# Optimization experiments

Hardware: AMD Instinct MI355X
Metric: run time of the kernel (lower is better)

## Reference

```python
import jax, jax.numpy as jnp
import numpy as np

EPS = 1e-5

def conv3(x, w, b):
    # 3x3 conv, stride 1, pad 1, NCHW/OIHW
    y = jax.lax.conv_general_dilated(x, w, (1, 1), ((1, 1), (1, 1)),
                                     dimension_numbers=('NCHW', 'OIHW', 'NCHW'))
    return y + b[None, :, None, None]

def positional_norm(x):
    # per-pixel channel-wise norm; torch .var() is unbiased (ddof=1)
    mean = jnp.mean(x, axis=1, keepdims=True)
    var = jnp.var(x, axis=1, keepdims=True, ddof=1)
    return (x - mean) / jnp.sqrt(var + EPS)

def bilinear_gather(x, py, px):
    # x: [B,C,H,W]; py/px: [B,K,H,W] absolute sample coords -> [B,C,K,H,W]
    B, C, H, W = x.shape
    K = py.shape[1]
    xf = x.reshape(B, C, H * W)
    y0 = jnp.floor(py).astype(jnp.int32)
    x0 = jnp.floor(px).astype(jnp.int32)
    wy = py - y0.astype(x.dtype)
    wx = px - x0.astype(x.dtype)

    def corner(yi, xi):
        valid = ((yi >= 0) & (yi < H) & (xi >= 0) & (xi < W)).astype(x.dtype)
        idx = (jnp.clip(yi, 0, H - 1) * W + jnp.clip(xi, 0, W - 1)).reshape(B, 1, K * H * W)
        v = jnp.take_along_axis(xf, idx, axis=2).reshape(B, C, K, H, W)
        return v * valid[:, None]

    out = ((1 - wy) * (1 - wx))[:, None] * corner(y0, x0)
    out = out + ((1 - wy) * wx)[:, None] * corner(y0, x0 + 1)
    out = out + (wy * (1 - wx))[:, None] * corner(y0 + 1, x0)
    out = out + (wy * wx)[:, None] * corner(y0 + 1, x0 + 1)
    return out

def dcn_v2(feat, cond, w_off, b_off, w_dcn, b_dcn):
    # DCNv2Pack: conv_offset(cond) -> (o1, o2, mask); modulated deformable 3x3 conv on feat
    B, C, H, W = feat.shape
    om = conv3(cond, w_off, b_off)                      # [B, 27, H, W]
    off = om[:, :18].reshape(B, 9, 2, H, W)             # (dy, dx) per kernel tap
    mask = jax.nn.sigmoid(om[:, 18:])                   # [B, 9, H, W]
    dy, dx = off[:, :, 0], off[:, :, 1]
    ki = jnp.repeat(jnp.arange(-1.0, 2.0, dtype=feat.dtype), 3)   # tap row offsets
    kj = jnp.tile(jnp.arange(-1.0, 2.0, dtype=feat.dtype), 3)     # tap col offsets
    hh = jnp.arange(H, dtype=feat.dtype)
    ww = jnp.arange(W, dtype=feat.dtype)
    py = dy + hh[None, None, :, None] + ki[None, :, None, None]
    px = dx + ww[None, None, None, :] + kj[None, :, None, None]
    sampled = bilinear_gather(feat, py, px)             # [B,C,9,H,W]
    wk = w_dcn.reshape(w_dcn.shape[0], C, 9)
    out = jnp.einsum('bkhw,bckhw,ock->bohw', mask, sampled, wk)
    return out + b_dcn[None, :, None, None]

def spade_forward(x, ref, w1, b1, w2, b2, w_off, b_off, w_dcn, b_dcn, w_g, b_g, w_be, b_be):
    normalized = positional_norm(x)
    h = jax.nn.relu(conv3(jnp.concatenate((normalized, ref), axis=1), w1, b1))
    cond = jax.nn.relu(conv3(h, w2, b2))
    ref_refine = dcn_v2(ref, cond, w_off, b_off, w_dcn, b_dcn)
    gamma = conv3(ref_refine, w_g, b_g)
    beta = conv3(ref_refine, w_be, b_be)
    return normalized * (1 + gamma) + beta

def setup_inputs() -> dict:
    key = jax.random.key(0)
    ks = jax.random.split(key, 16)
    B, NC, SC, H, W = 2, 64, 64, 96, 96
    mid = (NC + SC) // 8  # 16
    s = 0.05
    inp = {
        'x': jax.random.normal(ks[0], (B, NC, H, W), jnp.float32),
        'ref': jax.random.normal(ks[1], (B, SC, H, W), jnp.float32),
        'w1': jax.random.normal(ks[2], (mid, NC + SC, 3, 3), jnp.float32) * s,
        'b1': jax.random.normal(ks[3], (mid,), jnp.float32) * s,
        'w2': jax.random.normal(ks[4], (SC, mid, 3, 3), jnp.float32) * s,
        'b2': jax.random.normal(ks[5], (SC,), jnp.float32) * s,
        'w_off': jax.random.normal(ks[6], (27, SC, 3, 3), jnp.float32) * 0.01,
        'b_off': jax.random.normal(ks[7], (27,), jnp.float32) * 0.01,
        'w_dcn': jax.random.normal(ks[8], (SC, SC, 3, 3), jnp.float32) * s,
        'b_dcn': jax.random.normal(ks[9], (SC,), jnp.float32) * s,
        'w_g': jax.random.normal(ks[10], (NC, SC, 3, 3), jnp.float32) * s,
        'b_g': jax.random.normal(ks[11], (NC,), jnp.float32) * s,
        'w_be': jax.random.normal(ks[12], (NC, SC, 3, 3), jnp.float32) * s,
        'b_be': jax.random.normal(ks[13], (NC,), jnp.float32) * s,
    }
    return inp

def reference(x, ref, w1, b1, w2, b2, w_off, b_off, w_dcn, b_dcn, w_g, b_g, w_be, b_be):
    return spade_forward(x, ref, w1, b1, w2, b2, w_off, b_off, w_dcn, b_dcn, w_g, b_g, w_be, b_be)
```

## Files before the change

kernel.cpp:

```cpp
#include <hip/hip_runtime.h>
#include <math.h>

namespace {

typedef __attribute__((ext_vector_type(8))) short          bf16x8;
typedef __attribute__((ext_vector_type(8))) unsigned short u16x8;
typedef __attribute__((ext_vector_type(8))) _Float16       f16x8;
typedef __attribute__((ext_vector_type(4))) float          f32x4;

constexpr int B_  = 2;
constexpr int H_  = 96;
constexpr int W_  = 96;
constexpr int HW_ = H_ * W_;
constexpr int NC_ = 64;
constexpr int SC_ = 64;

__device__ inline unsigned short f2bf(float f) {
    union { float f; unsigned u; } v; v.f = f;
    unsigned r = v.u + 0x7FFFu + ((v.u >> 16) & 1u);
    return (unsigned short)(r >> 16);
}
__device__ inline unsigned short f2hbits(float f) {
    union { _Float16 h; unsigned short u; } s; s.h = (_Float16)f; return s.u;
}
__device__ inline _Float16 hfrombits(unsigned short u) {
    union { _Float16 h; unsigned short u; } s; s.u = u; return s.h;
}
__device__ inline bf16x8 ld_frag(const unsigned short* p) {
    return *reinterpret_cast<const bf16x8*>(p);
}

__global__ __launch_bounds__(256)
void prologue(const float* __restrict__ x, const float* __restrict__ ref,
              const float* __restrict__ w1, const float* __restrict__ w2,
              const float* __restrict__ woff, const float* __restrict__ wg,
              const float* __restrict__ wbe, const float* __restrict__ wdcn,
              float* __restrict__ nrm, unsigned short* __restrict__ cc,
              unsigned short* __restrict__ ccH,
              unsigned short* __restrict__ wt1, unsigned short* __restrict__ wt2,
              unsigned short* __restrict__ wtoff, unsigned short* __restrict__ wtg,
              unsigned short* __restrict__ wtbe, unsigned short* __restrict__ wbdH) {
    __shared__ float red1[4][64];
    __shared__ float red2[4][64];
    __shared__ float rtile[64][65];

    int blk = blockIdx.x;
    int t   = threadIdx.x;

    if (blk < 288) {
        int b  = blk / 144;
        int p0 = (blk % 144) * 64;
        int px = t & 63;
        int cg = t >> 6;
        int p  = p0 + px;

        float v[16];
        float s1 = 0.f, s2 = 0.f;
        const float* xb = x + ((size_t)b * NC_ + cg * 16) * HW_ + p;
        #pragma unroll
        for (int j = 0; j < 16; ++j) {
            v[j] = xb[j * HW_];
            s1 += v[j];
            s2 = fmaf(v[j], v[j], s2);
        }
        red1[cg][px] = s1;
        red2[cg][px] = s2;

        const float* rb = ref + (size_t)b * SC_ * HW_ + p0 + px;
        #pragma unroll
        for (int it = 0; it < 16; ++it) {
            int ch = it * 4 + cg;
            rtile[ch][px] = rb[(size_t)ch * HW_];
        }
        __syncthreads();

        s1 = red1[0][px] + red1[1][px] + red1[2][px] + red1[3][px];
        s2 = red2[0][px] + red2[1][px] + red2[2][px] + red2[3][px];
        float mean = s1 * (1.f / 64.f);
        float var  = (s2 - 64.f * mean * mean) * (1.f / 63.f);
        float inv  = 1.f / sqrtf(var + 1e-5f);
        float* nb = nrm + ((size_t)b * NC_ + cg * 16) * HW_ + p;
        u16x8 pk[2];
        #pragma unroll
        for (int j = 0; j < 16; ++j) {
            float nv = (v[j] - mean) * inv;
            nb[j * HW_] = nv;
            pk[j >> 3][j & 7] = f2bf(nv);
        }
        size_t bp = (size_t)b * HW_ + p;
        *reinterpret_cast<u16x8*>(&cc[bp * 128 + cg * 16 + 0]) = pk[0];
        *reinterpret_cast<u16x8*>(&cc[bp * 128 + cg * 16 + 8]) = pk[1];

        {
            int wpx = t >> 2, q = t & 3;
            size_t bp2 = (size_t)b * HW_ + p0 + wpx;
            u16x8 o0, o1, h0, h1;
            #pragma unroll
            for (int j = 0; j < 8; ++j) {
                float v0 = rtile[q * 16 + j][wpx];
                float v1 = rtile[q * 16 + 8 + j][wpx];
                o0[j] = f2bf(v0);    o1[j] = f2bf(v1);
                h0[j] = f2hbits(v0); h1[j] = f2hbits(v1);
            }
            *reinterpret_cast<u16x8*>(&cc[bp2 * 128 + 64 + q * 16 + 0]) = o0;
            *reinterpret_cast<u16x8*>(&cc[bp2 * 128 + 64 + q * 16 + 8]) = o1;
            *reinterpret_cast<u16x8*>(&ccH[bp2 * 64 + q * 16 + 0]) = h0;
            *reinterpret_cast<u16x8*>(&ccH[bp2 * 64 + q * 16 + 8]) = h1;
        }
    } else {
        int idx = (blk - 288) * 256 + t;
        if (idx < 9 * 16 * 128) {
            int tap = idx / (16 * 128), oc = (idx / 128) % 16, ic = idx % 128;
            wt1[idx] = f2bf(w1[(oc * 128 + ic) * 9 + tap]);
        }
        if (idx < 9 * 64 * 32) {
            int tap = idx / (64 * 32), oc = (idx / 32) % 64, ic = idx % 32;
            wt2[idx] = (ic < 16) ? f2bf(w2[(oc * 16 + ic) * 9 + tap]) : (unsigned short)0;
        }
        if (idx < 9 * 32 * 64) {
            int tap = idx / (32 * 64), oc = (idx / 64) % 32, ic = idx % 64;
            wtoff[idx] = (oc < 27) ? f2bf(woff[(oc * 64 + ic) * 9 + tap]) : (unsigned short)0;
        }
        if (idx < 9 * 64 * 64) {
            int tap = idx / (64 * 64), oc = (idx / 64) % 64, ic = idx % 64;
            wtg[idx]  = f2bf(wg [(oc * 64 + ic) * 9 + tap]);
            wtbe[idx] = f2bf(wbe[(oc * 64 + ic) * 9 + tap]);
        }
        if (idx < 64 * 576) {
            int oc = idx / 576, r = idx - oc * 576;
            int tap = r >> 6, ic = r & 63;
            wbdH[idx] = f2hbits(wdcn[oc * 576 + ic * 9 + tap]);
        }
    }
}

template <int ICS, int ICP, int COLP, int COUT_PAD, int COUT_REAL,
          bool DUAL, bool RELU, int OMODE>
__global__ __launch_bounds__(256)
void conv_bf(const unsigned short* __restrict__ in,
             const unsigned short* __restrict__ Wt,
             const unsigned short* __restrict__ Wt2,
             const float* __restrict__ bias, const float* __restrict__ bias2,
             const float* __restrict__ nrm, float* __restrict__ outF,
             unsigned short* __restrict__ outB) {
    constexpr int NOCT = COUT_PAD / 16;
    constexpr int WPO  = 4 / NOCT;
    constexpr int MTP  = NOCT;
    constexpr int NACC = DUAL ? 2 : 1;
    constexpr int NKS  = ICP / 32;
    constexpr int NCH8 = ICP / 8;

    __shared__ unsigned short patch[6 * 18 * COLP];

    int t   = threadIdx.x;
    int blk = blockIdx.x;
    int bx  = blk % 6;
    int by  = (blk / 6) % 24;
    int b   = blk / 144;
    int x0  = bx * 16, y0 = by * 4;

    for (int e = t; e < 6 * 18 * NCH8; e += 256) {
        int kc  = e % NCH8;
        int col = (e / NCH8) % 18;
        int row = e / (NCH8 * 18);
        int yy = y0 + row - 1, xx = x0 + col - 1;
        bf16x8 v = (bf16x8){0, 0, 0, 0, 0, 0, 0, 0};
        if (kc * 8 < ICS && (unsigned)yy < (unsigned)H_ && (unsigned)xx < (unsigned)W_) {
            v = ld_frag(&in[((size_t)b * HW_ + yy * W_ + xx) * ICS + kc * 8]);
        }
        *reinterpret_cast<bf16x8*>(&patch[(row * 18 + col) * COLP + kc * 8]) = v;
    }
    __syncthreads();

    int wave = t >> 6, lane = t & 63;
    int fr = lane & 15, fq = lane >> 4;
    int oct  = wave / WPO;
    int widx = wave - oct * WPO;
    int mt0  = widx * MTP;

    f32x4 acc[MTP][NACC];
    #pragma unroll
    for (int i = 0; i < MTP; ++i)
        #pragma unroll
        for (int a = 0; a < NACC; ++a)
            acc[i][a] = (f32x4){0.f, 0.f, 0.f, 0.f};

    constexpr int dyv[9] = {0,0,0,1,1,1,2,2,2};
    constexpr int dxv[9] = {0,1,2,0,1,2,0,1,2};

    #pragma unroll
    for (int tap = 0; tap < 9; ++tap) {
        int dy = dyv[tap], dx = dxv[tap];
        #pragma unroll
        for (int ks = 0; ks < NKS; ++ks) {
            const size_t wo = ((size_t)tap * COUT_PAD + oct * 16 + fr) * ICP + ks * 32 + fq * 8;
            bf16x8 wfA = ld_frag(&Wt[wo]);
            bf16x8 wfB;
            if (DUAL) wfB = ld_frag(&Wt2[wo]);
            #pragma unroll
            for (int i = 0; i < MTP; ++i) {
                bf16x8 pf = ld_frag(&patch[((mt0 + i + dy) * 18 + (fr + dx)) * COLP
                                           + ks * 32 + fq * 8]);
                acc[i][0] = __builtin_amdgcn_mfma_f32_16x16x32_bf16(wfA, pf, acc[i][0], 0, 0, 0);
                if (DUAL)
                    acc[i][1] = __builtin_amdgcn_mfma_f32_16x16x32_bf16(wfB, pf, acc[i][1], 0, 0, 0);
            }
        }
    }

    #pragma unroll
    for (int i = 0; i < MTP; ++i) {
        int py = mt0 + i;
        if (OMODE == 1) {
            size_t p = (size_t)b * HW_ + (size_t)(y0 + py) * W_ + x0 + fr;
            ushort4 sv;
            #pragma unroll
            for (int j = 0; j < 4; ++j) {
                float v = acc[i][0][j] + bias[oct * 16 + fq * 4 + j];
                if (RELU) v = fmaxf(v, 0.f);
                ((unsigned short*)&sv)[j] = f2bf(v);
            }
            *reinterpret_cast<ushort4*>(&outB[p * COUT_REAL + oct * 16 + fq * 4]) = sv;
        } else {
            #pragma unroll
            for (int j = 0; j < 4; ++j) {
                int oc = oct * 16 + fq * 4 + j;
                if (oc >= COUT_REAL) continue;
                size_t off = ((size_t)b * COUT_REAL + oc) * HW_
                           + (size_t)(y0 + py) * W_ + x0 + fr;
                float v = acc[i][0][j] + bias[oc];
                if (DUAL) {
                    float be = acc[i][1][j] + bias2[oc];
                    float nv = nrm[off];
                    outF[off] = fmaf(nv, 1.f + v, be);
                } else {
                    outF[off] = RELU ? fmaxf(v, 0.f) : v;
                }
            }
        }
    }
}

constexpr int SROW = 584;
constexpr int DT   = 32;

__global__ __launch_bounds__(256)
void dcn_kernel(const unsigned short* __restrict__ ccH,
                const unsigned short* __restrict__ condT,
                const unsigned short* __restrict__ wtoff,
                const float* __restrict__ b_off,
                const unsigned short* __restrict__ wbdH,
                const float* __restrict__ b_dcn,
                unsigned short* __restrict__ rrT) {
    __shared__ unsigned short uS[DT * SROW];
    __shared__ float  omL[DT][36];
    __shared__ ushort4 cwLh[DT * 9];
    __shared__ int4    ciL[DT * 9];

    int t = threadIdx.x;
    int bid = blockIdx.x;
    int swz = (bid & 7) * 72 + (bid >> 3);
    int b   = swz / (HW_ / DT);
    int p0  = (swz % (HW_ / DT)) * DT;
    int y   = p0 / W_, x0 = p0 - y * W_;

    for (int e = t; e < 3 * 34 * 8; e += 256) {
        int kc  = e & 7;
        int col = (e >> 3) % 34;
        int row = (e >> 3) / 34;
        int yy = y + row - 1, xx = x0 + col - 1;
        bf16x8 v = (bf16x8){0, 0, 0, 0, 0, 0, 0, 0};
        if ((unsigned)yy < (unsigned)H_ && (unsigned)xx < (unsigned)W_) {
            v = ld_frag(&condT[((size_t)b * HW_ + yy * W_ + xx) * 64 + kc * 8]);
        }
        *reinterpret_cast<bf16x8*>(&uS[(row * 34 + col) * 72 + kc * 8]) = v;
    }
    __syncthreads();

    int wave = t >> 6, lane = t & 63;
    int fr = lane & 15, fq = lane >> 4;

    {
        int oct = wave & 1, mt = wave >> 1;
        f32x4 acc = (f32x4){0.f, 0.f, 0.f, 0.f};
        constexpr int dyv[9] = {0,0,0,1,1,1,2,2,2};
        constexpr int dxv[9] = {0,1,2,0,1,2,0,1,2};
        #pragma unroll
        for (int tap = 0; tap < 9; ++tap) {
            int dy = dyv[tap], dx = dxv[tap];
            #pragma unroll
            for (int ks = 0; ks < 2; ++ks) {
                bf16x8 wf = ld_frag(&wtoff[((size_t)tap * 32 + oct * 16 + fr) * 64
                                           + ks * 32 + fq * 8]);
                bf16x8 pf = *reinterpret_cast<const bf16x8*>(
                    &uS[(dy * 34 + mt * 16 + fr + dx) * 72 + ks * 32 + fq * 8]);
                acc = __builtin_amdgcn_mfma_f32_16x16x32_bf16(wf, pf, acc, 0, 0, 0);
            }
        }
        int px = mt * 16 + fr;
        float4 o4;
        #pragma unroll
        for (int j = 0; j < 4; ++j) {
            int oc = oct * 16 + fq * 4 + j;
            ((float*)&o4)[j] = acc[j] + (oc < 27 ? b_off[oc] : 0.f);
        }
        *reinterpret_cast<float4*>(&omL[px][oct * 16 + fq * 4]) = o4;
    }
    __syncthreads();

    for (int e = t; e < DT * 9; e += 256) {
        int pp = e / 9, k = e - pp * 9;
        int p  = p0 + pp;
        int yq = p / W_, xq = p - yq * W_;
        float dy = omL[pp][2 * k];
        float dx = omL[pp][2 * k + 1];
        float mk = omL[pp][18 + k];
        mk = 1.f / (1.f + expf(-mk));

        float py = dy + (float)yq + (float)(k / 3 - 1);
        float px = dx + (float)xq + (float)(k % 3 - 1);
        float fy = floorf(py), fx = floorf(px);
        int   y0 = (int)fy,   x0c = (int)fx;
        float wy = py - fy,   wx = px - fx;

        ushort4 cwh;
        int   ci[4];
        #pragma unroll
        for (int i = 0; i < 4; ++i) {
            int yy = y0 + (i >> 1);
            int xx = x0c + (i & 1);
            bool valid = (yy >= 0) && (yy < H_) && (xx >= 0) && (xx < W_);
            int yc = yy < 0 ? 0 : (yy > H_ - 1 ? H_ - 1 : yy);
            int xc = xx < 0 ? 0 : (xx > W_ - 1 ? W_ - 1 : xx);
            ci[i] = yc * W_ + xc;
            float wyi = (i >> 1) ? wy : (1.f - wy);
            float wxi = (i & 1)  ? wx : (1.f - wx);
            ((unsigned short*)&cwh)[i] = f2hbits(valid ? mk * wyi * wxi : 0.f);
        }
        cwLh[e] = cwh;
        ciL[e] = make_int4(ci[0], ci[1], ci[2], ci[3]);
    }
    __syncthreads();

    {
        const unsigned short* ch = ccH + (size_t)b * HW_ * 64;
        int pp = t >> 3, cg8 = t & 7;
        #pragma unroll
        for (int k = 0; k < 9; ++k) {
            ushort4 cwh = cwLh[pp * 9 + k];
            int4    ci  = ciL[pp * 9 + k];
            f16x8 r0 = *reinterpret_cast<const f16x8*>(&ch[(size_t)ci.x * 64 + cg8 * 8]);
            f16x8 r1 = *reinterpret_cast<const f16x8*>(&ch[(size_t)ci.y * 64 + cg8 * 8]);
            f16x8 r2 = *reinterpret_cast<const f16x8*>(&ch[(size_t)ci.z * 64 + cg8 * 8]);
            f16x8 r3 = *reinterpret_cast<const f16x8*>(&ch[(size_t)ci.w * 64 + cg8 * 8]);
            _Float16 h0 = hfrombits(cwh.x);
            _Float16 h1 = hfrombits(cwh.y);
            _Float16 h2 = hfrombits(cwh.z);
            _Float16 h3 = hfrombits(cwh.w);
            f16x8 s = r0 * h0;
            s += r1 * h1;
            s += r2 * h2;
            s += r3 * h3;
            *reinterpret_cast<f16x8*>(&uS[pp * SROW + k * 64 + cg8 * 8]) = s;
        }
    }
    __syncthreads();

    f32x4 acc0 = (f32x4){0.f, 0.f, 0.f, 0.f};
    f32x4 acc1 = (f32x4){0.f, 0.f, 0.f, 0.f};
    for (int ks = 0; ks < 18; ++ks) {
        f16x8 wf  = *reinterpret_cast<const f16x8*>(
            &wbdH[(size_t)(wave * 16 + fr) * 576 + ks * 32 + fq * 8]);
        f16x8 pf0 = *reinterpret_cast<const f16x8*>(
            &uS[(size_t)fr * SROW + ks * 32 + fq * 8]);
        f16x8 pf1 = *reinterpret_cast<const f16x8*>(
            &uS[(size_t)(16 + fr) * SROW + ks * 32 + fq * 8]);
        acc0 = __builtin_amdgcn_mfma_f32_16x16x32_f16(wf, pf0, acc0, 0, 0, 0);
        acc1 = __builtin_amdgcn_mfma_f32_16x16x32_f16(wf, pf1, acc1, 0, 0, 0);
    }

    {
        size_t p = (size_t)b * HW_ + p0 + fr;
        ushort4 sv0, sv1;
        #pragma unroll
        for (int j = 0; j < 4; ++j) {
            float bo = b_dcn[wave * 16 + fq * 4 + j];
            ((unsigned short*)&sv0)[j] = f2bf(acc0[j] + bo);
            ((unsigned short*)&sv1)[j] = f2bf(acc1[j] + bo);
        }
        *reinterpret_cast<ushort4*>(&rrT[p * 64 + wave * 16 + fq * 4]) = sv0;
        *reinterpret_cast<ushort4*>(&rrT[(p + 16) * 64 + wave * 16 + fq * 4]) = sv1;
    }
}

}

extern "C" void kernel_launch(void* const* d_in, const int* in_sizes, int n_in,
                              void* d_out, int out_size, void* d_ws, size_t ws_size,
                              hipStream_t stream) {
    (void)in_sizes; (void)n_in; (void)out_size; (void)ws_size;

    const float* x     = (const float*)d_in[0];
    const float* ref   = (const float*)d_in[1];
    const float* w1    = (const float*)d_in[2];
    const float* b1    = (const float*)d_in[3];
    const float* w2    = (const float*)d_in[4];
    const float* b2    = (const float*)d_in[5];
    const float* w_off = (const float*)d_in[6];
    const float* b_off = (const float*)d_in[7];
    const float* w_dcn = (const float*)d_in[8];
    const float* b_dcn = (const float*)d_in[9];
    const float* w_g   = (const float*)d_in[10];
    const float* b_g   = (const float*)d_in[11];
    const float* w_be  = (const float*)d_in[12];
    const float* b_be  = (const float*)d_in[13];

    float* out = (float*)d_out;
    float* ws  = (float*)d_ws;

    float* nrm = ws;
    unsigned short* cc    = (unsigned short*)(nrm + 1179648);
    unsigned short* ccH   = cc    + 2359296;
    unsigned short* hmidT = ccH   + 1179648;
    unsigned short* condT = hmidT + 294912;
    unsigned short* rrT   = condT + 1179648;
    unsigned short* wt1   = rrT   + 1179648;
    unsigned short* wt2   = wt1   + 18432;
    unsigned short* wtoff = wt2   + 18432;
    unsigned short* wtg   = wtoff + 18432;
    unsigned short* wtbe  = wtg   + 36864;
    unsigned short* wbdH  = wtbe  + 36864;

    prologue<<<432, 256, 0, stream>>>(x, ref, w1, w2, w_off, w_g, w_be, w_dcn,
                                      nrm, cc, ccH, wt1, wt2, wtoff, wtg, wtbe, wbdH);

    constexpr int GRID = 288;

    conv_bf<128, 128, 136, 16, 16, false, true, 1>
        <<<GRID, 256, 0, stream>>>(cc, wt1, nullptr, b1, nullptr, nullptr, nullptr, hmidT);

    conv_bf<16, 32, 40, 64, 64, false, true, 1>
        <<<GRID, 256, 0, stream>>>(hmidT, wt2, nullptr, b2, nullptr, nullptr, nullptr, condT);

    dcn_kernel<<<B_ * (HW_ / DT), 256, 0, stream>>>(ccH, condT, wtoff, b_off,
                                                    wbdH, b_dcn, rrT);

    conv_bf<64, 64, 72, 64, 64, true, false, 0>
        <<<GRID, 256, 0, stream>>>(rrT, wtg, wtbe, b_g, b_be, nrm, out, nullptr);
}
```

Before: 68.02 us.

## Fuse second shared conv into DCN kernel and halve final conv tile rows

The second 3x3 conv (hmid to cond) now runs inside the DCN kernel. Each block recomputes the cond halo tile from a 5x50 hmid patch in shared memory and feeds it straight into the offset conv, so the condT round trip through global memory and one kernel launch go away. In exchange, halo pixels are computed redundantly (3x48 conv outputs per block for 32 pixels). The conv kernel is also templated on rows per block, and the final gamma/beta conv uses 2-row tiles with a doubled grid for more parallelism.

```diff
diff --git a/kernel.cpp b/kernel.cpp
--- a/kernel.cpp
+++ b/kernel.cpp
@@ -134,7 +134,7 @@
     }
 }
 
-template <int ICS, int ICP, int COLP, int COUT_PAD, int COUT_REAL,
+template <int R, int ICS, int ICP, int COLP, int COUT_PAD, int COUT_REAL,
           bool DUAL, bool RELU, int OMODE>
 __global__ __launch_bounds__(256)
 void conv_bf(const unsigned short* __restrict__ in,
@@ -145,21 +145,23 @@
              unsigned short* __restrict__ outB) {
     constexpr int NOCT = COUT_PAD / 16;
     constexpr int WPO  = 4 / NOCT;
-    constexpr int MTP  = NOCT;
+    constexpr int MTP  = R / WPO;
     constexpr int NACC = DUAL ? 2 : 1;
     constexpr int NKS  = ICP / 32;
     constexpr int NCH8 = ICP / 8;
-
-    __shared__ unsigned short patch[6 * 18 * COLP];
+    constexpr int TY   = 96 / R;
+    constexpr int PR   = R + 2;
+
+    __shared__ unsigned short patch[PR * 18 * COLP];
 
     int t   = threadIdx.x;
     int blk = blockIdx.x;
     int bx  = blk % 6;
-    int by  = (blk / 6) % 24;
-    int b   = blk / 144;
-    int x0  = bx * 16, y0 = by * 4;
-
-    for (int e = t; e < 6 * 18 * NCH8; e += 256) {
+    int by  = (blk / 6) % TY;
+    int b   = blk / (6 * TY);
+    int x0  = bx * 16, y0 = by * R;
+
+    for (int e = t; e < PR * 18 * NCH8; e += 256) {
         int kc  = e % NCH8;
         int col = (e / NCH8) % 18;
         int row = e / (NCH8 * 18);
@@ -243,10 +245,14 @@
 
 constexpr int SROW = 584;
 constexpr int DT   = 32;
+constexpr int HMO  = 0;
+constexpr int CNO  = 8192;
 
 __global__ __launch_bounds__(256)
 void dcn_kernel(const unsigned short* __restrict__ ccH,
-                const unsigned short* __restrict__ condT,
+                const unsigned short* __restrict__ hmidT,
+                const unsigned short* __restrict__ wt2,
+                const float* __restrict__ b2,
                 const unsigned short* __restrict__ wtoff,
                 const float* __restrict__ b_off,
                 const unsigned short* __restrict__ wbdH,
@@ -264,21 +270,53 @@
     int p0  = (swz % (HW_ / DT)) * DT;
     int y   = p0 / W_, x0 = p0 - y * W_;
 
-    for (int e = t; e < 3 * 34 * 8; e += 256) {
-        int kc  = e & 7;
-        int col = (e >> 3) % 34;
-        int row = (e >> 3) / 34;
-        int yy = y + row - 1, xx = x0 + col - 1;
-        bf16x8 v = (bf16x8){0, 0, 0, 0, 0, 0, 0, 0};
-        if ((unsigned)yy < (unsigned)H_ && (unsigned)xx < (unsigned)W_) {
-            v = ld_frag(&condT[((size_t)b * HW_ + yy * W_ + xx) * 64 + kc * 8]);
-        }
-        *reinterpret_cast<bf16x8*>(&uS[(row * 34 + col) * 72 + kc * 8]) = v;
-    }
-    __syncthreads();
-
     int wave = t >> 6, lane = t & 63;
     int fr = lane & 15, fq = lane >> 4;
+
+    for (int e = t; e < 5 * 50 * 4; e += 256) {
+        int kc  = e & 3;
+        int col = (e >> 2) % 50;
+        int row = (e >> 2) / 50;
+        int yy = y + row - 2, xx = x0 + col - 2;
+        bf16x8 v = (bf16x8){0, 0, 0, 0, 0, 0, 0, 0};
+        if (kc < 2 && (unsigned)yy < (unsigned)H_ && (unsigned)xx < (unsigned)W_) {
+            v = ld_frag(&hmidT[((size_t)b * HW_ + yy * W_ + xx) * 16 + kc * 8]);
+        }
+        *reinterpret_cast<bf16x8*>(&uS[HMO + (row * 50 + col) * 32 + kc * 8]) = v;
+    }
+    __syncthreads();
+
+    {
+        constexpr int dyv[9] = {0,0,0,1,1,1,2,2,2};
+        constexpr int dxv[9] = {0,1,2,0,1,2,0,1,2};
+        int oct = wave;
+        #pragma unroll
+        for (int mt = 0; mt < 9; ++mt) {
+            int mr = mt / 3, mc = mt - mr * 3;
+            int c  = mc * 16 + fr;
+            f32x4 acc = (f32x4){0.f, 0.f, 0.f, 0.f};
+            #pragma unroll
+            for (int tap = 0; tap < 9; ++tap) {
+                bf16x8 wf = ld_frag(&wt2[((size_t)tap * 64 + oct * 16 + fr) * 32 + fq * 8]);
+                bf16x8 pf = *reinterpret_cast<const bf16x8*>(
+                    &uS[HMO + ((mr + dyv[tap]) * 50 + c + dxv[tap]) * 32 + fq * 8]);
+                acc = __builtin_amdgcn_mfma_f32_16x16x32_bf16(wf, pf, acc, 0, 0, 0);
+            }
+            if (c < 34) {
+                int gy = y - 1 + mr, gx = x0 - 1 + c;
+                bool inimg = ((unsigned)gy < (unsigned)H_) && ((unsigned)gx < (unsigned)W_);
+                ushort4 sv;
+                #pragma unroll
+                for (int j = 0; j < 4; ++j) {
+                    int oc = oct * 16 + fq * 4 + j;
+                    float v = inimg ? fmaxf(acc[j] + b2[oc], 0.f) : 0.f;
+                    ((unsigned short*)&sv)[j] = f2bf(v);
+                }
+                *reinterpret_cast<ushort4*>(&uS[CNO + (mr * 34 + c) * 72 + oct * 16 + fq * 4]) = sv;
+            }
+        }
+    }
+    __syncthreads();
 
     {
         int oct = wave & 1, mt = wave >> 1;
@@ -293,7 +331,7 @@
                 bf16x8 wf = ld_frag(&wtoff[((size_t)tap * 32 + oct * 16 + fr) * 64
                                            + ks * 32 + fq * 8]);
                 bf16x8 pf = *reinterpret_cast<const bf16x8*>(
-                    &uS[(dy * 34 + mt * 16 + fr + dx) * 72 + ks * 32 + fq * 8]);
+                    &uS[CNO + (dy * 34 + mt * 16 + fr + dx) * 72 + ks * 32 + fq * 8]);
                 acc = __builtin_amdgcn_mfma_f32_16x16x32_bf16(wf, pf, acc, 0, 0, 0);
             }
         }
@@ -320,14 +358,14 @@
         float py = dy + (float)yq + (float)(k / 3 - 1);
         float px = dx + (float)xq + (float)(k % 3 - 1);
         float fy = floorf(py), fx = floorf(px);
-        int   y0 = (int)fy,   x0c = (int)fx;
+        int   y0c = (int)fy,  x0c = (int)fx;
         float wy = py - fy,   wx = px - fx;
 
         ushort4 cwh;
         int   ci[4];
         #pragma unroll
         for (int i = 0; i < 4; ++i) {
-            int yy = y0 + (i >> 1);
+            int yy = y0c + (i >> 1);
             int xx = x0c + (i & 1);
             bool valid = (yy >= 0) && (yy < H_) && (xx >= 0) && (xx < W_);
             int yc = yy < 0 ? 0 : (yy > H_ - 1 ? H_ - 1 : yy);
@@ -422,8 +460,7 @@
     unsigned short* cc    = (unsigned short*)(nrm + 1179648);
     unsigned short* ccH   = cc    + 2359296;
     unsigned short* hmidT = ccH   + 1179648;
-    unsigned short* condT = hmidT + 294912;
-    unsigned short* rrT   = condT + 1179648;
+    unsigned short* rrT   = hmidT + 294912;
     unsigned short* wt1   = rrT   + 1179648;
     unsigned short* wt2   = wt1   + 18432;
     unsigned short* wtoff = wt2   + 18432;
@@ -434,17 +471,12 @@
     prologue<<<432, 256, 0, stream>>>(x, ref, w1, w2, w_off, w_g, w_be, w_dcn,
                                       nrm, cc, ccH, wt1, wt2, wtoff, wtg, wtbe, wbdH);
 
-    constexpr int GRID = 288;
-
-    conv_bf<128, 128, 136, 16, 16, false, true, 1>
-        <<<GRID, 256, 0, stream>>>(cc, wt1, nullptr, b1, nullptr, nullptr, nullptr, hmidT);
-
-    conv_bf<16, 32, 40, 64, 64, false, true, 1>
-        <<<GRID, 256, 0, stream>>>(hmidT, wt2, nullptr, b2, nullptr, nullptr, nullptr, condT);
-
-    dcn_kernel<<<B_ * (HW_ / DT), 256, 0, stream>>>(ccH, condT, wtoff, b_off,
-                                                    wbdH, b_dcn, rrT);
-
-    conv_bf<64, 64, 72, 64, 64, true, false, 0>
-        <<<GRID, 256, 0, stream>>>(rrT, wtg, wtbe, b_g, b_be, nrm, out, nullptr);
-}
+    conv_bf<4, 128, 128, 136, 16, 16, false, true, 1>
+        <<<288, 256, 0, stream>>>(cc, wt1, nullptr, b1, nullptr, nullptr, nullptr, hmidT);
+
+    dcn_kernel<<<B_ * (HW_ / DT), 256, 0, stream>>>(ccH, hmidT, wt2, b2,
+                                                    wtoff, b_off, wbdH, b_dcn, rrT);
+
+    conv_bf<2, 64, 64, 72, 64, 64, true, false, 0>
+        <<<576, 256, 0, stream>>>(rrT, wtg, wtbe, b_g, b_be, nrm, out, nullptr);
+}
```

Result: no change. 68.59 us (+0.8%).

## Drop fp32 normalized buffer, reuse bf16 copy; halve final conv tile rows

Applied to the files above, without the earlier changes.

The prologue no longer writes the fp32 positional-norm tensor. The final SPADE modulation conv instead reads the normalized value from the existing bf16 concatenated buffer, which removes a full fp32 write and read of the activation. The conv kernel now takes a rows-per-block template parameter, and the last gamma/beta conv uses 2 rows per block on 576 blocks to spread work across more CUs. Using the bf16 normalized value in the output reduces precision of the x_norm term, and the smaller tiles add more halo reloads.

```diff
diff --git a/kernel.cpp b/kernel.cpp
--- a/kernel.cpp
+++ b/kernel.cpp
@@ -20,6 +20,9 @@
     unsigned r = v.u + 0x7FFFu + ((v.u >> 16) & 1u);
     return (unsigned short)(r >> 16);
 }
+__device__ inline float bf2f(unsigned short s) {
+    union { unsigned u; float f; } v; v.u = ((unsigned)s) << 16; return v.f;
+}
 __device__ inline unsigned short f2hbits(float f) {
     union { _Float16 h; unsigned short u; } s; s.h = (_Float16)f; return s.u;
 }
@@ -35,8 +38,7 @@
               const float* __restrict__ w1, const float* __restrict__ w2,
               const float* __restrict__ woff, const float* __restrict__ wg,
               const float* __restrict__ wbe, const float* __restrict__ wdcn,
-              float* __restrict__ nrm, unsigned short* __restrict__ cc,
-              unsigned short* __restrict__ ccH,
+              unsigned short* __restrict__ cc, unsigned short* __restrict__ ccH,
               unsigned short* __restrict__ wt1, unsigned short* __restrict__ wt2,
               unsigned short* __restrict__ wtoff, unsigned short* __restrict__ wtg,
               unsigned short* __restrict__ wtbe, unsigned short* __restrict__ wbdH) {
@@ -79,12 +81,10 @@
         float mean = s1 * (1.f / 64.f);
         float var  = (s2 - 64.f * mean * mean) * (1.f / 63.f);
         float inv  = 1.f / sqrtf(var + 1e-5f);
-        float* nb = nrm + ((size_t)b * NC_ + cg * 16) * HW_ + p;
         u16x8 pk[2];
         #pragma unroll
         for (int j = 0; j < 16; ++j) {
             float nv = (v[j] - mean) * inv;
-            nb[j * HW_] = nv;
             pk[j >> 3][j & 7] = f2bf(nv);
         }
         size_t bp = (size_t)b * HW_ + p;
@@ -134,32 +134,33 @@
     }
 }
 
-template <int ICS, int ICP, int COLP, int COUT_PAD, int COUT_REAL,
+template <int R, int ICS, int ICP, int COLP, int COUT_PAD, int COUT_REAL,
           bool DUAL, bool RELU, int OMODE>
 __global__ __launch_bounds__(256)
 void conv_bf(const unsigned short* __restrict__ in,
              const unsigned short* __restrict__ Wt,
              const unsigned short* __restrict__ Wt2,
              const float* __restrict__ bias, const float* __restrict__ bias2,
-             const float* __restrict__ nrm, float* __restrict__ outF,
+             const unsigned short* __restrict__ ccn, float* __restrict__ outF,
              unsigned short* __restrict__ outB) {
     constexpr int NOCT = COUT_PAD / 16;
     constexpr int WPO  = 4 / NOCT;
-    constexpr int MTP  = NOCT;
-    constexpr int NACC = DUAL ? 2 : 1;
+    constexpr int MTP  = R / WPO;
     constexpr int NKS  = ICP / 32;
     constexpr int NCH8 = ICP / 8;
-
-    __shared__ unsigned short patch[6 * 18 * COLP];
+    constexpr int TY   = 96 / R;
+    constexpr int PR   = R + 2;
+
+    __shared__ unsigned short patch[PR * 18 * COLP];
 
     int t   = threadIdx.x;
     int blk = blockIdx.x;
     int bx  = blk % 6;
-    int by  = (blk / 6) % 24;
-    int b   = blk / 144;
-    int x0  = bx * 16, y0 = by * 4;
-
-    for (int e = t; e < 6 * 18 * NCH8; e += 256) {
+    int by  = (blk / 6) % TY;
+    int b   = blk / (6 * TY);
+    int x0  = bx * 16, y0 = by * R;
+
+    for (int e = t; e < PR * 18 * NCH8; e += 256) {
         int kc  = e % NCH8;
         int col = (e / NCH8) % 18;
         int row = e / (NCH8 * 18);
@@ -178,12 +179,12 @@
     int widx = wave - oct * WPO;
     int mt0  = widx * MTP;
 
-    f32x4 acc[MTP][NACC];
+    f32x4 accA[MTP], accB[MTP];
     #pragma unroll
-    for (int i = 0; i < MTP; ++i)
-        #pragma unroll
-        for (int a = 0; a < NACC; ++a)
-            acc[i][a] = (f32x4){0.f, 0.f, 0.f, 0.f};
+    for (int i = 0; i < MTP; ++i) {
+        accA[i] = (f32x4){0.f, 0.f, 0.f, 0.f};
+        accB[i] = (f32x4){0.f, 0.f, 0.f, 0.f};
+    }
 
     constexpr int dyv[9] = {0,0,0,1,1,1,2,2,2};
     constexpr int dxv[9] = {0,1,2,0,1,2,0,1,2};
@@ -201,9 +202,9 @@
             for (int i = 0; i < MTP; ++i) {
                 bf16x8 pf = ld_frag(&patch[((mt0 + i + dy) * 18 + (fr + dx)) * COLP
                                            + ks * 32 + fq * 8]);
-                acc[i][0] = __builtin_amdgcn_mfma_f32_16x16x32_bf16(wfA, pf, acc[i][0], 0, 0, 0);
+                accA[i] = __builtin_amdgcn_mfma_f32_16x16x32_bf16(wfA, pf, accA[i], 0, 0, 0);
                 if (DUAL)
-                    acc[i][1] = __builtin_amdgcn_mfma_f32_16x16x32_bf16(wfB, pf, acc[i][1], 0, 0, 0);
+                    accB[i] = __builtin_amdgcn_mfma_f32_16x16x32_bf16(wfB, pf, accB[i], 0, 0, 0);
             }
         }
     }
@@ -216,22 +217,26 @@
             ushort4 sv;
             #pragma unroll
             for (int j = 0; j < 4; ++j) {
-                float v = acc[i][0][j] + bias[oct * 16 + fq * 4 + j];
+                float v = accA[i][j] + bias[oct * 16 + fq * 4 + j];
                 if (RELU) v = fmaxf(v, 0.f);
                 ((unsigned short*)&sv)[j] = f2bf(v);
             }
             *reinterpret_cast<ushort4*>(&outB[p * COUT_REAL + oct * 16 + fq * 4]) = sv;
         } else {
+            size_t pix = (size_t)b * HW_ + (size_t)(y0 + py) * W_ + x0 + fr;
+            ushort4 nv4;
+            if (DUAL)
+                nv4 = *reinterpret_cast<const ushort4*>(&ccn[pix * 128 + oct * 16 + fq * 4]);
             #pragma unroll
             for (int j = 0; j < 4; ++j) {
                 int oc = oct * 16 + fq * 4 + j;
                 if (oc >= COUT_REAL) continue;
                 size_t off = ((size_t)b * COUT_REAL + oc) * HW_
                            + (size_t)(y0 + py) * W_ + x0 + fr;
-                float v = acc[i][0][j] + bias[oc];
+                float v = accA[i][j] + bias[oc];
                 if (DUAL) {
-                    float be = acc[i][1][j] + bias2[oc];
-                    float nv = nrm[off];
+                    float be = accB[i][j] + bias2[oc];
+                    float nv = bf2f(((unsigned short*)&nv4)[j]);
                     outF[off] = fmaf(nv, 1.f + v, be);
                 } else {
                     outF[off] = RELU ? fmaxf(v, 0.f) : v;
@@ -320,14 +325,14 @@
         float py = dy + (float)yq + (float)(k / 3 - 1);
         float px = dx + (float)xq + (float)(k % 3 - 1);
         float fy = floorf(py), fx = floorf(px);
-        int   y0 = (int)fy,   x0c = (int)fx;
+        int   y0c = (int)fy,  x0c = (int)fx;
         float wy = py - fy,   wx = px - fx;
 
         ushort4 cwh;
         int   ci[4];
         #pragma unroll
         for (int i = 0; i < 4; ++i) {
-            int yy = y0 + (i >> 1);
+            int yy = y0c + (i >> 1);
             int xx = x0c + (i & 1);
             bool valid = (yy >= 0) && (yy < H_) && (xx >= 0) && (xx < W_);
             int yc = yy < 0 ? 0 : (yy > H_ - 1 ? H_ - 1 : yy);
@@ -416,10 +421,8 @@
     const float* b_be  = (const float*)d_in[13];
 
     float* out = (float*)d_out;
-    float* ws  = (float*)d_ws;
-
-    float* nrm = ws;
-    unsigned short* cc    = (unsigned short*)(nrm + 1179648);
+
+    unsigned short* cc    = (unsigned short*)d_ws;
     unsigned short* ccH   = cc    + 2359296;
     unsigned short* hmidT = ccH   + 1179648;
     unsigned short* condT = hmidT + 294912;
@@ -432,19 +435,16 @@
     unsigned short* wbdH  = wtbe  + 36864;
 
     prologue<<<432, 256, 0, stream>>>(x, ref, w1, w2, w_off, w_g, w_be, w_dcn,
-                                      nrm, cc, ccH, wt1, wt2, wtoff, wtg, wtbe, wbdH);
-
-    constexpr int GRID = 288;
-
-    conv_bf<128, 128, 136, 16, 16, false, true, 1>
-        <<<GRID, 256, 0, stream>>>(cc, wt1, nullptr, b1, nullptr, nullptr, nullptr, hmidT);
-
-    conv_bf<16, 32, 40, 64, 64, false, true, 1>
-        <<<GRID, 256, 0, stream>>>(hmidT, wt2, nullptr, b2, nullptr, nullptr, nullptr, condT);
-
-    dcn_kernel<<<B_ * (HW_ / DT), 256, 0, stream>>>(ccH, condT, wtoff, b_off,
-                                                    wbdH, b_dcn, rrT);
-
-    conv_bf<64, 64, 72, 64, 64, true, false, 0>
-        <<<GRID, 256, 0, stream>>>(rrT, wtg, wtbe, b_g, b_be, nrm, out, nullptr);
-}
+                                      cc, ccH, wt1, wt2, wtoff, wtg, wtbe, wbdH);
+
+    conv_bf<4, 128, 128, 136, 16, 16, false, true, 1>
+        <<<288, 256, 0, stream>>>(cc, wt1, nullptr, b1, nullptr, nullptr, nullptr, hmidT);
+
+    conv_bf<4, 16, 32, 40, 64, 64, false, true, 1>
+        <<<288, 256, 0, stream>>>(hmidT, wt2, nullptr, b2, nullptr, nullptr, nullptr, condT);
+
+    dcn_kernel<<<576, 256, 0, stream>>>(ccH, condT, wtoff, b_off, wbdH, b_dcn, rrT);
+
+    conv_bf<2, 64, 64, 72, 64, 64, true, false, 0>
+        <<<576, 256, 0, stream>>>(rrT, wtg, wtbe, b_g, b_be, cc, out, nullptr);
+}
```

Result: no change. 67.66 us (median of 2 runs) (-0.5%).
